# Optimization experiments

Measured on AMD Instinct MI355X. Metric: run time of the kernel, lower is better.

The kernel has to match this reference:

```python
import jax, jax.numpy as jnp
import numpy as np

INNER_DIM = 1024

def setup_inputs() -> dict:
    key = jax.random.key(0)
    ks = jax.random.split(key, 6)
    b, n, d = 4, 4096, 1024
    s = 0.02
    return {
        "x": jax.random.normal(ks[0], (b, n, d), jnp.float32),
        "y": jax.random.normal(ks[1], (b, n, d), jnp.float32),
        "Wq": jax.random.normal(ks[2], (INNER_DIM, d), jnp.float32) * s,
        "Wk": jax.random.normal(ks[3], (INNER_DIM, d), jnp.float32) * s,
        "Wv": jax.random.normal(ks[4], (INNER_DIM, d), jnp.float32) * s,
        "Wo": jax.random.normal(ks[5], (d, INNER_DIM), jnp.float32) * s,
        "bo": jnp.zeros((d,), jnp.float32),
    }

def reference(x, y, Wq, Wk, Wv, Wo, bo):
    # torch Linear: out = inp @ W.T ; weights stored [out_dim, in_dim]
    q = jnp.einsum('bnd,ed->bne', y, Wq)  # queries come from y
    k = jnp.einsum('bnd,ed->bne', x, Wk)
    v = jnp.einsum('bnd,ed->bne', x, Wv)
    dk = 1.0 / jnp.sqrt(jnp.asarray(INNER_DIM, q.dtype))  # full inner_dim, not per-head
    alpha = jnp.einsum('bie,bje->bij', q, k) * dk  # [b, n, n] full score matrix
    alpha = jax.nn.softmax(alpha, axis=-1)
    # NOTE: original masked_fill is a no-op (result discarded), so no causal mask.
    ctx = jnp.einsum('bij,bje->bie', alpha, v)
    return jnp.einsum('bie,de->bid', ctx, Wo) + bo
```

## Files before the change

### kernel.cpp

```cpp
#include <hip/hip_runtime.h>
#include <stdint.h>

typedef __attribute__((ext_vector_type(8))) short s16x8;
typedef __attribute__((ext_vector_type(4))) float f32x4;

__device__ __forceinline__ unsigned short f2bf(float f) {
    union { float f; uint32_t u; } c; c.f = f;
    uint32_t u = c.u + 0x7FFFu + ((c.u >> 16) & 1u);
    return (unsigned short)(u >> 16);
}

__device__ __forceinline__ float bf2f(unsigned int u16) {
    union { uint32_t u; float f; } c; c.u = u16 << 16;
    return c.f;
}

__device__ __forceinline__ void load_lds16(const unsigned short* g, unsigned short* l) {
    __builtin_amdgcn_global_load_lds(
        (const __attribute__((address_space(1))) char*)(uintptr_t)g,
        (__attribute__((address_space(3))) char*)(uint32_t)(uintptr_t)l,
        16, 0, 0);
}

__device__ __forceinline__ void gemm256_core(
    const unsigned short* __restrict__ Ap, long lda,
    const unsigned short* __restrict__ Bp, long ldb,
    int nt, unsigned short* As, unsigned short* Bs, f32x4 (*acc)[2])
{
    const int tid  = threadIdx.x;
    const int wv   = tid >> 6;
    const int lane = tid & 63;
    const int cl   = lane & 15;
    const int qd   = lane >> 4;

    const int ch0 = (wv << 7) + lane, ch1 = ch0 + 64;
    const int r0 = ch0 >> 3, r1 = ch1 >> 3;
    const long gA0 = (long)r0 * lda + (((ch0 & 7) ^ (r0 & 7)) << 3);
    const long gA1 = (long)r1 * lda + (((ch1 & 7) ^ (r1 & 7)) << 3);
    const long gB0 = (long)r0 * ldb + (((ch0 & 7) ^ (r0 & 7)) << 3);
    const long gB1 = (long)r1 * ldb + (((ch1 & 7) ^ (r1 & 7)) << 3);
    const int  d0  = (wv << 10);
    const int  d1  = d0 + 512;

    const int k0off = (((qd    ) ^ (cl & 7)) << 3) + cl * 64;
    const int k1off = (((4 + qd) ^ (cl & 7)) << 3) + cl * 64;

    load_lds16(Bp + gB0, Bs + d0);
    load_lds16(Bp + gB1, Bs + d1);
    load_lds16(Bp + 128 * ldb + gB0, Bs + 8192 + d0);
    load_lds16(Bp + 128 * ldb + gB1, Bs + 8192 + d1);
    load_lds16(Ap + gA0, As + d0);
    load_lds16(Ap + gA1, As + d1);
    load_lds16(Ap + 128 * lda + gA0, As + 8192 + d0);
    load_lds16(Ap + 128 * lda + gA1, As + 8192 + d1);
    asm volatile("s_waitcnt vmcnt(2)" ::: "memory");
    asm volatile("s_barrier" ::: "memory");

    for (int t = 0; t < nt; ++t) {
        const unsigned short* Ab = As + ((t & 1) << 14);
        const unsigned short* Bb = Bs + ((t & 1) << 14);
        unsigned short* An = As + (((t + 1) & 1) << 14);
        unsigned short* Bn = Bs + (((t + 1) & 1) << 14);
        const long kn   = (long)(t + 1) << 6;
        const bool more = (t + 1) < nt;
        s16x8 bfr[2][2];
#pragma unroll
        for (int p = 0; p < 4; ++p) {
            s16x8 af[4][2];
#pragma unroll
            for (int i = 0; i < 4; ++i) {
                af[i][0] = *(const s16x8*)&Ab[(p * 4 + i) * 1024 + k0off];
                af[i][1] = *(const s16x8*)&Ab[(p * 4 + i) * 1024 + k1off];
            }
            if (p == 0) {
#pragma unroll
                for (int j = 0; j < 2; ++j) {
                    bfr[j][0] = *(const s16x8*)&Bb[(wv * 2 + j) * 1024 + k0off];
                    bfr[j][1] = *(const s16x8*)&Bb[(wv * 2 + j) * 1024 + k1off];
                }
            }
            if (more) {
                if (p == 0)      { load_lds16(Bp + kn + gB0, Bn + d0);
                                   load_lds16(Bp + kn + gB1, Bn + d1); }
                else if (p == 1) { load_lds16(Bp + 128 * ldb + kn + gB0, Bn + 8192 + d0);
                                   load_lds16(Bp + 128 * ldb + kn + gB1, Bn + 8192 + d1); }
                else if (p == 2) { load_lds16(Ap + kn + gA0, An + d0);
                                   load_lds16(Ap + kn + gA1, An + d1); }
                else             { load_lds16(Ap + 128 * lda + kn + gA0, An + 8192 + d0);
                                   load_lds16(Ap + 128 * lda + kn + gA1, An + 8192 + d1); }
            }
            __builtin_amdgcn_s_setprio(1);
#pragma unroll
            for (int i = 0; i < 4; ++i)
#pragma unroll
                for (int j = 0; j < 2; ++j) {
                    acc[p * 4 + i][j] = __builtin_amdgcn_mfma_f32_16x16x32_bf16(
                        af[i][0], bfr[j][0], acc[p * 4 + i][j], 0, 0, 0);
                    acc[p * 4 + i][j] = __builtin_amdgcn_mfma_f32_16x16x32_bf16(
                        af[i][1], bfr[j][1], acc[p * 4 + i][j], 0, 0, 0);
                }
            __builtin_amdgcn_s_setprio(0);
            if (p == 1) {
                if (more) asm volatile("s_waitcnt vmcnt(4)" ::: "memory");
                else      asm volatile("s_waitcnt vmcnt(0)" ::: "memory");
            } else if (p == 3) {
                if (more) asm volatile("s_waitcnt vmcnt(2)" ::: "memory");
            }
            asm volatile("s_barrier" ::: "memory");
        }
    }
}

template <bool OUT_BF16, bool HAS_BIAS, bool EXP_OUT>
__global__ __launch_bounds__(512, 2)
void gemm256(const unsigned short* __restrict__ A, long lda, long sA,
             const unsigned short* __restrict__ B, long ldb, long sB,
             void* __restrict__ C, long ldc, long sC,
             const float* __restrict__ bias, int K, float scale)
{
    __shared__ __align__(16) unsigned short As[2 * 16384];
    __shared__ __align__(16) unsigned short Bs[2 * 16384];

    const unsigned gx = gridDim.x, gy = gridDim.y;
    const unsigned lin = blockIdx.x + gx * blockIdx.y;
    unsigned bxs, bys;
    if ((gy & 7u) == 0u) {
        const unsigned g = lin & 7u, j = lin >> 3;
        bxs = j & (gx - 1u);
        bys = g * (gy >> 3) + j / gx;
    } else { bxs = blockIdx.x; bys = blockIdx.y; }

    const unsigned short* Ap = A + (long)blockIdx.z * sA + (long)bys * 256 * lda;
    const unsigned short* Bp = B + (long)blockIdx.z * sB + (long)bxs * 256 * ldb;

    f32x4 acc[16][2];
#pragma unroll
    for (int i = 0; i < 16; ++i) {
        acc[i][0] = f32x4{0.f, 0.f, 0.f, 0.f};
        acc[i][1] = f32x4{0.f, 0.f, 0.f, 0.f};
    }

    gemm256_core(Ap, lda, Bp, ldb, K >> 6, As, Bs, acc);

    const int wv = threadIdx.x >> 6;
    const int cl = threadIdx.x & 15, qd = (threadIdx.x & 63) >> 4;
    const long row0 = (long)bys * 256;
    const long col0 = (long)bxs * 256 + wv * 32;
    const long zC   = (long)blockIdx.z * sC;
#pragma unroll
    for (int j = 0; j < 2; ++j) {
        const long c = col0 + j * 16 + cl;
        float badd = 0.f;
        if constexpr (HAS_BIAS) badd = bias[c];
#pragma unroll
        for (int i = 0; i < 16; ++i) {
            const long rb = row0 + i * 16 + qd * 4;
#pragma unroll
            for (int r = 0; r < 4; ++r) {
                float v = acc[i][j][r] * scale + badd;
                if constexpr (EXP_OUT) v = __expf(v);
                const long idx = zC + (rb + r) * ldc + c;
                if constexpr (OUT_BF16) ((unsigned short*)C)[idx] = f2bf(v);
                else                    ((float*)C)[idx] = v;
            }
        }
    }
}

__global__ __launch_bounds__(512, 2)
void gemm256_pv4(const unsigned short* __restrict__ p0,
                 const unsigned short* __restrict__ p1,
                 const unsigned short* __restrict__ p2,
                 const unsigned short* __restrict__ p3,
                 const unsigned short* __restrict__ Bv, long ldb, long sB,
                 unsigned short* __restrict__ C, long ldc, long sC,
                 const float* __restrict__ rowdiv, int K, long lda)
{
    __shared__ __align__(16) unsigned short As[2 * 16384];
    __shared__ __align__(16) unsigned short Bs[2 * 16384];

    const unsigned gx = gridDim.x, gy = gridDim.y;
    const unsigned lin = blockIdx.x + gx * blockIdx.y;
    unsigned bxs, bys;
    if ((gy & 7u) == 0u) {
        const unsigned g = lin & 7u, j = lin >> 3;
        bxs = j & (gx - 1u);
        bys = g * (gy >> 3) + j / gx;
    } else { bxs = blockIdx.x; bys = blockIdx.y; }

    const int z = blockIdx.z;
    const unsigned short* A = (z == 0) ? p0 : (z == 1) ? p1 : (z == 2) ? p2 : p3;

    const unsigned short* Ap = A + (long)bys * 256 * lda;
    const unsigned short* Bp = Bv + (long)z * sB + (long)bxs * 256 * ldb;

    f32x4 acc[16][2];
#pragma unroll
    for (int i = 0; i < 16; ++i) {
        acc[i][0] = f32x4{0.f, 0.f, 0.f, 0.f};
        acc[i][1] = f32x4{0.f, 0.f, 0.f, 0.f};
    }

    gemm256_core(Ap, lda, Bp, ldb, K >> 6, As, Bs, acc);

    const int wv = threadIdx.x >> 6;
    const int cl = threadIdx.x & 15, qd = (threadIdx.x & 63) >> 4;
    const long row0 = (long)bys * 256;
    const long col0 = (long)bxs * 256 + wv * 32;
    const long zC   = (long)z * sC;
    const float* rd = rowdiv + (long)z * 4096;
#pragma unroll
    for (int i = 0; i < 16; ++i) {
        const long rb = row0 + i * 16 + qd * 4;
        float rinv[4];
#pragma unroll
        for (int r = 0; r < 4; ++r) rinv[r] = 1.f / rd[rb + r];
#pragma unroll
        for (int j = 0; j < 2; ++j) {
            const long c = col0 + j * 16 + cl;
#pragma unroll
            for (int r = 0; r < 4; ++r)
                C[zC + (rb + r) * ldc + c] = f2bf(acc[i][j][r] * rinv[r]);
        }
    }
}

__global__ __launch_bounds__(256)
void rowsum4(const unsigned short* __restrict__ p0,
             const unsigned short* __restrict__ p1,
             const unsigned short* __restrict__ p2,
             const unsigned short* __restrict__ p3,
             float* __restrict__ rs)
{
    const unsigned row = blockIdx.x;
    const unsigned b = row >> 12;
    const unsigned short* P = (b == 0) ? p0 : (b == 1) ? p1 : (b == 2) ? p2 : p3;
    const long r = row & 4095u;
    const int tid = threadIdx.x, lane = tid & 63, wave = tid >> 6;

    const uint4* src = (const uint4*)(P + r * 4096);
    uint4 u0 = src[tid], u1 = src[tid + 256];
    float s = 0.f;
    {
        const unsigned* a = (const unsigned*)&u0;
        const unsigned* c = (const unsigned*)&u1;
#pragma unroll
        for (int i = 0; i < 4; ++i) {
            s += bf2f(a[i] & 0xFFFFu) + bf2f(a[i] >> 16);
            s += bf2f(c[i] & 0xFFFFu) + bf2f(c[i] >> 16);
        }
    }
#pragma unroll
    for (int off = 32; off > 0; off >>= 1) s += __shfl_xor(s, off);
    __shared__ float red[4];
    if (lane == 0) red[wave] = s;
    __syncthreads();
    if (tid == 0) rs[row] = red[0] + red[1] + red[2] + red[3];
}

__global__ __launch_bounds__(256)
void cast2_bf16(const float* __restrict__ s0, unsigned short* __restrict__ d0,
                const float* __restrict__ s1, unsigned short* __restrict__ d1)
{
    const float*    in  = blockIdx.y ? s1 : s0;
    unsigned short* out = blockIdx.y ? d1 : d0;
    const long i = ((long)blockIdx.x * 256 + threadIdx.x) * 4;
    const float4 v = *(const float4*)(in + i);
    ushort4 o;
    o.x = f2bf(v.x); o.y = f2bf(v.y); o.z = f2bf(v.z); o.w = f2bf(v.w);
    *(ushort4*)(out + i) = o;
}

__global__ __launch_bounds__(256)
void cast4_bf16(const float* __restrict__ s0, unsigned short* __restrict__ d0,
                const float* __restrict__ s1, unsigned short* __restrict__ d1,
                const float* __restrict__ s2, unsigned short* __restrict__ d2,
                const float* __restrict__ s3, unsigned short* __restrict__ d3)
{
    const float* in; unsigned short* out;
    switch (blockIdx.y) {
        case 0: in = s0; out = d0; break;
        case 1: in = s1; out = d1; break;
        case 2: in = s2; out = d2; break;
        default: in = s3; out = d3; break;
    }
    const long i = ((long)blockIdx.x * 256 + threadIdx.x) * 4;
    const float4 v = *(const float4*)(in + i);
    ushort4 o;
    o.x = f2bf(v.x); o.y = f2bf(v.y); o.z = f2bf(v.z); o.w = f2bf(v.w);
    *(ushort4*)(out + i) = o;
}

extern "C" void kernel_launch(void* const* d_in, const int* in_sizes, int n_in,
                              void* d_out, int out_size, void* d_ws, size_t ws_size,
                              hipStream_t stream)
{
    (void)in_sizes; (void)n_in; (void)out_size;
    const float* x  = (const float*)d_in[0];
    const float* y  = (const float*)d_in[1];
    const float* Wq = (const float*)d_in[2];
    const float* Wk = (const float*)d_in[3];
    const float* Wv = (const float*)d_in[4];
    const float* Wo = (const float*)d_in[5];
    const float* bo = (const float*)d_in[6];
    float* out = (float*)d_out;

    const long N = 4096, D = 1024;
    const long NB = N * D;
    const size_t MiB = 1ull << 20;
    const float dk = 0.03125f;
    char* w = (char*)d_ws;

    if (ws_size >= 200 * MiB) {
        unsigned short* Xb  = (unsigned short*)(w);
        unsigned short* Yb  = (unsigned short*)(w + 32 * MiB);
        unsigned short* Qb  = (unsigned short*)(w + 64 * MiB);
        unsigned short* Kb  = (unsigned short*)(w + 96 * MiB);
        unsigned short* VT  = (unsigned short*)(w + 128 * MiB);
        unsigned short* Wqb = (unsigned short*)(w + 192 * MiB);
        unsigned short* Wkb = (unsigned short*)(w + 194 * MiB);
        unsigned short* Wvb = (unsigned short*)(w + 196 * MiB);
        unsigned short* Wob = (unsigned short*)(w + 198 * MiB);
        unsigned short* P0  = (unsigned short*)(w);
        unsigned short* P1  = (unsigned short*)(w + 32 * MiB);
        unsigned short* P2  = (unsigned short*)(w + 160 * MiB);
        unsigned short* P3  = (unsigned short*)d_out;
        unsigned short* Cx  = (unsigned short*)(w + 64 * MiB);
        float*          rsm = (float*)(w + 192 * MiB);

        cast2_bf16<<<dim3(16384, 2), dim3(256), 0, stream>>>(x, Xb, y, Yb);
        cast4_bf16<<<dim3(1024, 4),  dim3(256), 0, stream>>>(
            Wq, Wqb, Wk, Wkb, Wv, Wvb, Wo, Wob);

        gemm256<true, false, false><<<dim3(4, 64, 2), dim3(512), 0, stream>>>(
            Yb, D, (long)(Xb - Yb), Wqb, D, (long)(Wkb - Wqb),
            Qb, D, (long)(Kb - Qb), nullptr, (int)D, 1.f);
        gemm256<true, false, false><<<dim3(16, 4, 4), dim3(512), 0, stream>>>(
            Wvb, D, 0, Xb, D, NB, VT, N, NB, nullptr, (int)D, 1.f);

        gemm256<true, false, true><<<dim3(16, 16, 2), dim3(512), 0, stream>>>(
            Qb, D, NB, Kb, D, NB, P0, N, (long)(P1 - P0), nullptr, (int)D, dk);
        gemm256<true, false, true><<<dim3(16, 16, 2), dim3(512), 0, stream>>>(
            Qb + 2 * NB, D, NB, Kb + 2 * NB, D, NB,
            P2, N, (long)(P3 - P2), nullptr, (int)D, dk);
        rowsum4<<<dim3(16384), dim3(256), 0, stream>>>(P0, P1, P2, P3, rsm);

        gemm256_pv4<<<dim3(4, 16, 4), dim3(512), 0, stream>>>(
            P0, P1, P2, P3, VT, N, NB, Cx, D, NB, rsm, (int)N, N);
        gemm256<false, true, false><<<dim3(4, 64, 1), dim3(512), 0, stream>>>(
            Cx, D, 0, Wob, D, 0, out, D, 0, bo, (int)D, 1.f);
    } else if (ws_size >= 104 * MiB) {
        unsigned short* Wqb = (unsigned short*)(w);
        unsigned short* Wkb = (unsigned short*)(w + 2 * MiB);
        unsigned short* Wvb = (unsigned short*)(w + 4 * MiB);
        unsigned short* Wob = (unsigned short*)(w + 6 * MiB);
        unsigned short* xb  = (unsigned short*)(w + 8 * MiB);
        unsigned short* yb  = (unsigned short*)(w + 16 * MiB);
        unsigned short* Qb  = (unsigned short*)(w + 24 * MiB);
        unsigned short* Kb  = (unsigned short*)(w + 32 * MiB);
        unsigned short* VTb = (unsigned short*)(w + 40 * MiB);
        unsigned short* Cxb = (unsigned short*)(w + 48 * MiB);
        unsigned short* Pb  = (unsigned short*)(w + 56 * MiB);
        float*          rsm = (float*)(w + 88 * MiB);

        cast4_bf16<<<dim3(1024, 4), dim3(256), 0, stream>>>(
            Wq, Wqb, Wk, Wkb, Wv, Wvb, Wo, Wob);

        for (int b = 0; b < 4; ++b) {
            cast2_bf16<<<dim3(4096, 2), dim3(256), 0, stream>>>(
                x + b * NB, xb, y + b * NB, yb);
            gemm256<true, false, false><<<dim3(4, 16, 1), dim3(512), 0, stream>>>(
                yb, D, 0, Wqb, D, 0, Qb, D, 0, nullptr, (int)D, 1.f);
            gemm256<true, false, false><<<dim3(4, 16, 1), dim3(512), 0, stream>>>(
                xb, D, 0, Wkb, D, 0, Kb, D, 0, nullptr, (int)D, 1.f);
            gemm256<true, false, false><<<dim3(16, 4, 1), dim3(512), 0, stream>>>(
                Wvb, D, 0, xb, D, 0, VTb, N, 0, nullptr, (int)D, 1.f);
            gemm256<true, false, true><<<dim3(16, 16, 1), dim3(512), 0, stream>>>(
                Qb, D, 0, Kb, D, 0, Pb, N, 0, nullptr, (int)D, dk);
            rowsum4<<<dim3(4096), dim3(256), 0, stream>>>(Pb, Pb, Pb, Pb, rsm);
            gemm256_pv4<<<dim3(4, 16, 1), dim3(512), 0, stream>>>(
                Pb, Pb, Pb, Pb, VTb, N, 0, Cxb, D, 0, rsm, (int)N, N);
            gemm256<false, true, false><<<dim3(4, 16, 1), dim3(512), 0, stream>>>(
                Cxb, D, 0, Wob, D, 0, out + b * NB, D, 0, bo, (int)D, 1.f);
        }
    }
}
```

Measured before the change: 615.4 us.

## Tile waves as 2x4 grid over the 256x256 block instead of 1x8 columns

Each of the 8 waves now computes a 128x64 sub-tile (8x4 MFMA tiles) instead of a 256x32 strip. Per k-step a wave reads 8 A fragments and 4 B fragments from LDS rather than 16 and 2, which cuts LDS read traffic per MFMA. The global-to-LDS load mapping is reshuffled so each load phase fills the half of the tile consumed first. The accumulator count stays the same, but the epilogue write pattern and the wait/barrier timing relative to the new load order change.

```diff
diff --git a/kernel.cpp b/kernel.cpp
--- a/kernel.cpp
+++ b/kernel.cpp
@@ -25,34 +25,44 @@
 __device__ __forceinline__ void gemm256_core(
     const unsigned short* __restrict__ Ap, long lda,
     const unsigned short* __restrict__ Bp, long ldb,
-    int nt, unsigned short* As, unsigned short* Bs, f32x4 (*acc)[2])
+    int nt, unsigned short* As, unsigned short* Bs, f32x4 (*acc)[4])
 {
     const int tid  = threadIdx.x;
     const int wv   = tid >> 6;
     const int lane = tid & 63;
     const int cl   = lane & 15;
     const int qd   = lane >> 4;
-
-    const int ch0 = (wv << 7) + lane, ch1 = ch0 + 64;
-    const int r0 = ch0 >> 3, r1 = ch1 >> 3;
-    const long gA0 = (long)r0 * lda + (((ch0 & 7) ^ (r0 & 7)) << 3);
-    const long gA1 = (long)r1 * lda + (((ch1 & 7) ^ (r1 & 7)) << 3);
-    const long gB0 = (long)r0 * ldb + (((ch0 & 7) ^ (r0 & 7)) << 3);
-    const long gB1 = (long)r1 * ldb + (((ch1 & 7) ^ (r1 & 7)) << 3);
-    const int  d0  = (wv << 10);
-    const int  d1  = d0 + 512;
+    const int wm   = wv >> 2;
+    const int wn   = wv & 3;
+
+    long srcA[2][2], srcB[2][2];
+    int  dstL[2][2];
+#pragma unroll
+    for (int h = 0; h < 2; ++h) {
+#pragma unroll
+        for (int c = 0; c < 2; ++c) {
+            const int q0    = (wv << 7) + (c << 6);
+            const int phys0 = q0 + (q0 & 512) + (h << 9);
+            const int phys  = phys0 + lane;
+            const int g     = phys >> 3;
+            const long koff = (long)(((lane & 7) ^ (g & 7)) << 3);
+            srcA[h][c] = (long)g * lda + koff;
+            srcB[h][c] = (long)g * ldb + koff;
+            dstL[h][c] = phys0 << 3;
+        }
+    }
 
     const int k0off = (((qd    ) ^ (cl & 7)) << 3) + cl * 64;
     const int k1off = (((4 + qd) ^ (cl & 7)) << 3) + cl * 64;
 
-    load_lds16(Bp + gB0, Bs + d0);
-    load_lds16(Bp + gB1, Bs + d1);
-    load_lds16(Bp + 128 * ldb + gB0, Bs + 8192 + d0);
-    load_lds16(Bp + 128 * ldb + gB1, Bs + 8192 + d1);
-    load_lds16(Ap + gA0, As + d0);
-    load_lds16(Ap + gA1, As + d1);
-    load_lds16(Ap + 128 * lda + gA0, As + 8192 + d0);
-    load_lds16(Ap + 128 * lda + gA1, As + 8192 + d1);
+    load_lds16(Bp + srcB[0][0], Bs + dstL[0][0]);
+    load_lds16(Bp + srcB[0][1], Bs + dstL[0][1]);
+    load_lds16(Bp + srcB[1][0], Bs + dstL[1][0]);
+    load_lds16(Bp + srcB[1][1], Bs + dstL[1][1]);
+    load_lds16(Ap + srcA[0][0], As + dstL[0][0]);
+    load_lds16(Ap + srcA[0][1], As + dstL[0][1]);
+    load_lds16(Ap + srcA[1][0], As + dstL[1][0]);
+    load_lds16(Ap + srcA[1][1], As + dstL[1][1]);
     asm volatile("s_waitcnt vmcnt(2)" ::: "memory");
     asm volatile("s_barrier" ::: "memory");
 
@@ -63,41 +73,43 @@
         unsigned short* Bn = Bs + (((t + 1) & 1) << 14);
         const long kn   = (long)(t + 1) << 6;
         const bool more = (t + 1) < nt;
-        s16x8 bfr[2][2];
+        s16x8 bfr[4][2];
 #pragma unroll
         for (int p = 0; p < 4; ++p) {
-            s16x8 af[4][2];
-#pragma unroll
-            for (int i = 0; i < 4; ++i) {
-                af[i][0] = *(const s16x8*)&Ab[(p * 4 + i) * 1024 + k0off];
-                af[i][1] = *(const s16x8*)&Ab[(p * 4 + i) * 1024 + k1off];
+            s16x8 af[2][2];
+#pragma unroll
+            for (int i = 0; i < 2; ++i) {
+                const int s = (wm << 3) + (p << 1) + i;
+                af[i][0] = *(const s16x8*)&Ab[s * 1024 + k0off];
+                af[i][1] = *(const s16x8*)&Ab[s * 1024 + k1off];
             }
             if (p == 0) {
 #pragma unroll
-                for (int j = 0; j < 2; ++j) {
-                    bfr[j][0] = *(const s16x8*)&Bb[(wv * 2 + j) * 1024 + k0off];
-                    bfr[j][1] = *(const s16x8*)&Bb[(wv * 2 + j) * 1024 + k1off];
+                for (int j = 0; j < 4; ++j) {
+                    const int s = (wn << 2) + j;
+                    bfr[j][0] = *(const s16x8*)&Bb[s * 1024 + k0off];
+                    bfr[j][1] = *(const s16x8*)&Bb[s * 1024 + k1off];
                 }
             }
             if (more) {
-                if (p == 0)      { load_lds16(Bp + kn + gB0, Bn + d0);
-                                   load_lds16(Bp + kn + gB1, Bn + d1); }
-                else if (p == 1) { load_lds16(Bp + 128 * ldb + kn + gB0, Bn + 8192 + d0);
-                                   load_lds16(Bp + 128 * ldb + kn + gB1, Bn + 8192 + d1); }
-                else if (p == 2) { load_lds16(Ap + kn + gA0, An + d0);
-                                   load_lds16(Ap + kn + gA1, An + d1); }
-                else             { load_lds16(Ap + 128 * lda + kn + gA0, An + 8192 + d0);
-                                   load_lds16(Ap + 128 * lda + kn + gA1, An + 8192 + d1); }
+                if (p == 0)      { load_lds16(Bp + kn + srcB[0][0], Bn + dstL[0][0]);
+                                   load_lds16(Bp + kn + srcB[0][1], Bn + dstL[0][1]); }
+                else if (p == 1) { load_lds16(Bp + kn + srcB[1][0], Bn + dstL[1][0]);
+                                   load_lds16(Bp + kn + srcB[1][1], Bn + dstL[1][1]); }
+                else if (p == 2) { load_lds16(Ap + kn + srcA[0][0], An + dstL[0][0]);
+                                   load_lds16(Ap + kn + srcA[0][1], An + dstL[0][1]); }
+                else             { load_lds16(Ap + kn + srcA[1][0], An + dstL[1][0]);
+                                   load_lds16(Ap + kn + srcA[1][1], An + dstL[1][1]); }
             }
             __builtin_amdgcn_s_setprio(1);
 #pragma unroll
-            for (int i = 0; i < 4; ++i)
-#pragma unroll
-                for (int j = 0; j < 2; ++j) {
-                    acc[p * 4 + i][j] = __builtin_amdgcn_mfma_f32_16x16x32_bf16(
-                        af[i][0], bfr[j][0], acc[p * 4 + i][j], 0, 0, 0);
-                    acc[p * 4 + i][j] = __builtin_amdgcn_mfma_f32_16x16x32_bf16(
-                        af[i][1], bfr[j][1], acc[p * 4 + i][j], 0, 0, 0);
+            for (int i = 0; i < 2; ++i)
+#pragma unroll
+                for (int j = 0; j < 4; ++j) {
+                    acc[p * 2 + i][j] = __builtin_amdgcn_mfma_f32_16x16x32_bf16(
+                        af[i][0], bfr[j][0], acc[p * 2 + i][j], 0, 0, 0);
+                    acc[p * 2 + i][j] = __builtin_amdgcn_mfma_f32_16x16x32_bf16(
+                        af[i][1], bfr[j][1], acc[p * 2 + i][j], 0, 0, 0);
                 }
             __builtin_amdgcn_s_setprio(0);
             if (p == 1) {
@@ -133,27 +145,28 @@
     const unsigned short* Ap = A + (long)blockIdx.z * sA + (long)bys * 256 * lda;
     const unsigned short* Bp = B + (long)blockIdx.z * sB + (long)bxs * 256 * ldb;
 
-    f32x4 acc[16][2];
-#pragma unroll
-    for (int i = 0; i < 16; ++i) {
-        acc[i][0] = f32x4{0.f, 0.f, 0.f, 0.f};
-        acc[i][1] = f32x4{0.f, 0.f, 0.f, 0.f};
-    }
+    f32x4 acc[8][4];
+#pragma unroll
+    for (int i = 0; i < 8; ++i)
+#pragma unroll
+        for (int j = 0; j < 4; ++j)
+            acc[i][j] = f32x4{0.f, 0.f, 0.f, 0.f};
 
     gemm256_core(Ap, lda, Bp, ldb, K >> 6, As, Bs, acc);
 
     const int wv = threadIdx.x >> 6;
+    const int wm = wv >> 2, wn = wv & 3;
     const int cl = threadIdx.x & 15, qd = (threadIdx.x & 63) >> 4;
-    const long row0 = (long)bys * 256;
-    const long col0 = (long)bxs * 256 + wv * 32;
+    const long row0 = (long)bys * 256 + wm * 128;
+    const long col0 = (long)bxs * 256 + wn * 64;
     const long zC   = (long)blockIdx.z * sC;
 #pragma unroll
-    for (int j = 0; j < 2; ++j) {
+    for (int j = 0; j < 4; ++j) {
         const long c = col0 + j * 16 + cl;
         float badd = 0.f;
         if constexpr (HAS_BIAS) badd = bias[c];
 #pragma unroll
-        for (int i = 0; i < 16; ++i) {
+        for (int i = 0; i < 8; ++i) {
             const long rb = row0 + i * 16 + qd * 4;
 #pragma unroll
             for (int r = 0; r < 4; ++r) {
@@ -194,29 +207,30 @@
     const unsigned short* Ap = A + (long)bys * 256 * lda;
     const unsigned short* Bp = Bv + (long)z * sB + (long)bxs * 256 * ldb;
 
-    f32x4 acc[16][2];
-#pragma unroll
-    for (int i = 0; i < 16; ++i) {
-        acc[i][0] = f32x4{0.f, 0.f, 0.f, 0.f};
-        acc[i][1] = f32x4{0.f, 0.f, 0.f, 0.f};
-    }
+    f32x4 acc[8][4];
+#pragma unroll
+    for (int i = 0; i < 8; ++i)
+#pragma unroll
+        for (int j = 0; j < 4; ++j)
+            acc[i][j] = f32x4{0.f, 0.f, 0.f, 0.f};
 
     gemm256_core(Ap, lda, Bp, ldb, K >> 6, As, Bs, acc);
 
     const int wv = threadIdx.x >> 6;
+    const int wm = wv >> 2, wn = wv & 3;
     const int cl = threadIdx.x & 15, qd = (threadIdx.x & 63) >> 4;
-    const long row0 = (long)bys * 256;
-    const long col0 = (long)bxs * 256 + wv * 32;
+    const long row0 = (long)bys * 256 + wm * 128;
+    const long col0 = (long)bxs * 256 + wn * 64;
     const long zC   = (long)z * sC;
     const float* rd = rowdiv + (long)z * 4096;
 #pragma unroll
-    for (int i = 0; i < 16; ++i) {
+    for (int i = 0; i < 8; ++i) {
         const long rb = row0 + i * 16 + qd * 4;
         float rinv[4];
 #pragma unroll
         for (int r = 0; r < 4; ++r) rinv[r] = 1.f / rd[rb + r];
 #pragma unroll
-        for (int j = 0; j < 2; ++j) {
+        for (int j = 0; j < 4; ++j) {
             const long c = col0 + j * 16 + cl;
 #pragma unroll
             for (int r = 0; r < 4; ++r)
```

Result: slower. 640.0 us (+4.0%).
